# Performance work log

Measured on AMD Instinct MI355X. Metric: run time of the kernel, lower is better.

The kernel has to match this reference:

```python
import jax, jax.numpy as jnp
import numpy as np

N_NODES = 50000
N_EDGES = 800000
N_GRAPHS = 64
D = 90


def _kaiming_uniform(key, shape, fan_in):
    # kaiming_uniform_ with nonlinearity='relu': gain=sqrt(2), bound=gain*sqrt(3/fan_in)
    bound = np.sqrt(2.0) * np.sqrt(3.0 / fan_in)
    return jax.random.uniform(key, shape, jnp.float32, -bound, bound)


def setup_inputs() -> dict:
    key = jax.random.key(0)
    ks = jax.random.split(key, 16)
    x = jax.random.normal(ks[0], (N_NODES, D), jnp.float32)
    edge_index = jax.random.randint(ks[1], (2, N_EDGES), 0, N_NODES, jnp.int64)
    batch = jnp.sort(jax.random.randint(ks[2], (N_NODES,), 0, N_GRAPHS, jnp.int64))
    inp = {"x": x, "edge_index": edge_index, "batch": batch}
    # SAGEConv params: lin_l (neighbor path, with bias), lin_r (root path, no bias)
    for i, (kl, kr) in enumerate([(ks[3], ks[4]), (ks[5], ks[6]), (ks[7], ks[8])], start=1):
        inp[f"W{i}l"] = _kaiming_uniform(kl, (D, D), D)
        inp[f"b{i}"] = jnp.zeros((D,), jnp.float32)
        inp[f"W{i}r"] = _kaiming_uniform(kr, (D, D), D)
    inp["Wf1"] = _kaiming_uniform(ks[9], (32, D), D)
    inp["bf1"] = jnp.zeros((32,), jnp.float32)
    inp["Wf2"] = _kaiming_uniform(ks[10], (1, 32), 32)
    inp["bf2"] = jnp.zeros((1,), jnp.float32)
    return inp


def _sage_conv(x, src, dst, Wl, bl, Wr):
    # mean-aggregate neighbor messages x[src] at dst, then lin_l(agg) + lin_r(x)
    msg = x[src]                                           # [E, D] gather
    agg = jax.ops.segment_sum(msg, dst, num_segments=N_NODES)  # [N, D] scatter-add
    deg = jax.ops.segment_sum(jnp.ones((src.shape[0],), x.dtype), dst,
                              num_segments=N_NODES)
    agg = agg / jnp.maximum(deg, 1.0)[:, None]
    return agg @ Wl.T + bl + x @ Wr.T


def reference(x, edge_index, batch, W1l, b1, W1r, W2l, b2, W2r, W3l, b3, W3r,
              Wf1, bf1, Wf2, bf2):
    src, dst = edge_index[0], edge_index[1]
    h = jax.nn.relu(_sage_conv(x, src, dst, W1l, b1, W1r))
    h = jax.nn.relu(_sage_conv(h, src, dst, W2l, b2, W2r))
    h = jax.nn.relu(_sage_conv(h, src, dst, W3l, b3, W3r))
    # global_mean_pool over graph ids
    sums = jax.ops.segment_sum(h, batch, num_segments=N_GRAPHS)      # [G, D]
    cnts = jax.ops.segment_sum(jnp.ones((h.shape[0],), h.dtype), batch,
                               num_segments=N_GRAPHS)
    pooled = sums / jnp.maximum(cnts, 1.0)[:, None]
    h4 = jax.nn.relu(pooled @ Wf1.T + bf1)
    return h4 @ Wf2.T + bf2  # [G, 1]
```

## Files before the change

kernel.cpp:

```cpp
#include <hip/hip_runtime.h>
#include <hip/hip_bf16.h>

#define N_NODES 50000
#define N_PAD   50048
#define N_EDGES 800000
#define N_GRAPHS 64
#define D 90
#define SC  192
#define SCD 96

#define NBUCKETS 196
#define BSHIFT 8
#define BIN_EPB 4096

typedef __attribute__((ext_vector_type(8))) short bf16x8;
typedef __attribute__((ext_vector_type(4))) float f32x4;

__device__ __forceinline__ float bflo(unsigned int v) { return __uint_as_float(v << 16); }
__device__ __forceinline__ float bfhi(unsigned int v) { return __uint_as_float(v & 0xffff0000u); }
__device__ __forceinline__ unsigned short bf16bits(float f) {
    __hip_bfloat16 b = __float2bfloat16(f);
    return *(unsigned short*)&b;
}
__device__ __forceinline__ unsigned int pack2bf(float lo, float hi) {
    return (unsigned int)bf16bits(lo) | ((unsigned int)bf16bits(hi) << 16);
}

__global__ void k_prep(const float* __restrict__ x, __hip_bfloat16* __restrict__ cat,
                       const float* __restrict__ w1l, const float* __restrict__ w1r,
                       const float* __restrict__ w2l, const float* __restrict__ w2r,
                       const float* __restrict__ w3l, const float* __restrict__ w3r,
                       __hip_bfloat16* __restrict__ Wcat,
                       int* __restrict__ bcnt, float* __restrict__ pooled) {
    int idx = blockIdx.x * 256 + threadIdx.x;
    if (idx < N_PAD * 96) {
        int n = idx / 96, k = idx - n * 96;
        float v = (n < N_NODES && k < D) ? x[n * D + k] : 0.f;
        cat[n * SC + 96 + k] = __float2bfloat16(v);
    }
    if (idx < 3 * 96 * SC) {
        const int per = 96 * SC;
        int layer = idx / per, rem = idx - layer * per;
        int j = rem / SC, k = rem - j * SC;
        const float* wl = (layer == 0) ? w1l : (layer == 1) ? w2l : w3l;
        const float* wr = (layer == 0) ? w1r : (layer == 1) ? w2r : w3r;
        float v = 0.f;
        if (j < D) {
            if (k < 96) { if (k < D) v = wl[j * D + k]; }
            else        { int kk = k - 96; if (kk < D) v = wr[j * D + kk]; }
        }
        Wcat[idx] = __float2bfloat16(v);
    }
    if (idx < N_GRAPHS * D + N_GRAPHS) pooled[idx] = 0.f;
    if (idx < NBUCKETS) bcnt[idx] = 0;
}

__global__ void k_hist(const int* __restrict__ dst, int* __restrict__ bcnt) {
    __shared__ int h[NBUCKETS];
    int t = threadIdx.x;
    for (int i = t; i < NBUCKETS; i += 256) h[i] = 0;
    __syncthreads();
    int base = blockIdx.x * BIN_EPB;
    int lim = base + BIN_EPB; if (lim > N_EDGES) lim = N_EDGES;
    for (int e = base + t; e < lim; e += 256)
        atomicAdd(&h[dst[e] >> BSHIFT], 1);
    __syncthreads();
    for (int i = t; i < NBUCKETS; i += 256) {
        int c = h[i];
        if (c) atomicAdd(&bcnt[i], c);
    }
}

__global__ void k_bscan(const int* __restrict__ bcnt, int* __restrict__ bbase,
                        int* __restrict__ bcursor) {
    __shared__ int s[256];
    int t = threadIdx.x;
    int v = (t < NBUCKETS) ? bcnt[t] : 0;
    s[t] = v; __syncthreads();
    for (int o = 1; o < 256; o <<= 1) {
        int x = (t >= o) ? s[t - o] : 0;
        __syncthreads();
        s[t] += x;
        __syncthreads();
    }
    int excl = s[t] - v;
    if (t < NBUCKETS) { bbase[t] = excl; bcursor[t] = excl; }
    if (t == 255) bbase[NBUCKETS] = s[255];
}

__global__ __launch_bounds__(256) void k_bin(const int* __restrict__ src,
                                             const int* __restrict__ dst,
                                             int* __restrict__ bcursor,
                                             unsigned int* __restrict__ ebuf) {
    __shared__ int h[NBUCKETS];
    __shared__ int gb[NBUCKETS];
    int t = threadIdx.x;
    for (int i = t; i < NBUCKETS; i += 256) h[i] = 0;
    __syncthreads();
    int base = blockIdx.x * BIN_EPB;
    int sv[16], dv[16], rv[16];
    #pragma unroll
    for (int i = 0; i < 16; ++i) {
        int e = base + i * 256 + t;
        if (e < N_EDGES) {
            sv[i] = src[e];
            dv[i] = dst[e];
            rv[i] = atomicAdd(&h[dv[i] >> BSHIFT], 1);
        }
    }
    __syncthreads();
    for (int i = t; i < NBUCKETS; i += 256)
        gb[i] = h[i] ? atomicAdd(&bcursor[i], h[i]) : 0;
    __syncthreads();
    #pragma unroll
    for (int i = 0; i < 16; ++i) {
        int e = base + i * 256 + t;
        if (e < N_EDGES) {
            int b = dv[i] >> BSHIFT;
            ebuf[gb[b] + rv[i]] = (unsigned int)sv[i] | ((unsigned int)(dv[i] & 255) << 16);
        }
    }
}

__global__ __launch_bounds__(256) void k_fill2(const unsigned int* __restrict__ ebuf,
                                               const int* __restrict__ bbase,
                                               int* __restrict__ off,
                                               int* __restrict__ csr) {
    __shared__ int lcnt[256];
    __shared__ int excl[256];
    int t = threadIdx.x;
    int n0 = blockIdx.x << BSHIFT;
    int ebeg = bbase[blockIdx.x], eend = bbase[blockIdx.x + 1];
    lcnt[t] = 0;
    __syncthreads();
    for (int e = ebeg + t; e < eend; e += 256)
        atomicAdd(&lcnt[ebuf[e] >> 16], 1);
    __syncthreads();
    int v = lcnt[t];
    excl[t] = v; __syncthreads();
    for (int o = 1; o < 256; o <<= 1) {
        int x = (t >= o) ? excl[t - o] : 0;
        __syncthreads();
        excl[t] += x;
        __syncthreads();
    }
    excl[t] -= v;
    int n = n0 + t;
    if (n <= N_NODES) off[n] = ebeg + excl[t];
    lcnt[t] = 0;
    __syncthreads();
    for (int e = ebeg + t; e < eend; e += 256) {
        unsigned int u = ebuf[e];
        int li = u >> 16;
        int r = atomicAdd(&lcnt[li], 1);
        csr[ebeg + excl[li] + r] = (int)(u & 0xFFFFu);
    }
}

__global__ void k_agg(unsigned int* __restrict__ cat,
                      const int* __restrict__ off, const int* __restrict__ csr) {
    int wid  = (blockIdx.x * 256 + threadIdx.x) >> 6;
    int lane = threadIdx.x & 63;
    if (wid >= N_NODES) return;
    int beg = off[wid], end = off[wid + 1];
    int eg = lane >> 3, sl = lane & 7;
    int col = 48 + 6 * sl;

    float a[12];
    #pragma unroll
    for (int i = 0; i < 12; ++i) a[i] = 0.f;

    int e = beg + eg;
    for (; e + 8 < end; e += 16) {
        int sA = csr[e], sB = csr[e + 8];
        const unsigned int* pA = &cat[sA * SCD + col];
        const unsigned int* pB = &cat[sB * SCD + col];
        unsigned int u[6], v[6];
        #pragma unroll
        for (int i = 0; i < 6; ++i) u[i] = pA[i];
        #pragma unroll
        for (int i = 0; i < 6; ++i) v[i] = pB[i];
        #pragma unroll
        for (int i = 0; i < 6; ++i) {
            a[2 * i]     += bflo(u[i]) + bflo(v[i]);
            a[2 * i + 1] += bfhi(u[i]) + bfhi(v[i]);
        }
    }
    if (e < end) {
        const unsigned int* pA = &cat[csr[e] * SCD + col];
        unsigned int u[6];
        #pragma unroll
        for (int i = 0; i < 6; ++i) u[i] = pA[i];
        #pragma unroll
        for (int i = 0; i < 6; ++i) {
            a[2 * i]     += bflo(u[i]);
            a[2 * i + 1] += bfhi(u[i]);
        }
    }

    #pragma unroll
    for (int m = 8; m <= 32; m <<= 1) {
        #pragma unroll
        for (int i = 0; i < 12; ++i) a[i] += __shfl_xor(a[i], m);
    }

    if (eg == 0) {
        float inv = 1.0f / fmaxf((float)(end - beg), 1.0f);
        unsigned int* q = &cat[wid * SCD + 6 * sl];
        #pragma unroll
        for (int i = 0; i < 6; ++i) {
            int c0 = 12 * sl + 2 * i;
            float lo = (c0     < D) ? a[2 * i]     * inv : 0.f;
            float hi = (c0 + 1 < D) ? a[2 * i + 1] * inv : 0.f;
            q[i] = pack2bf(lo, hi);
        }
    }
}

__global__ __launch_bounds__(256) void k_gemm(
    const __hip_bfloat16* __restrict__ Acat,
    const __hip_bfloat16* __restrict__ Wcat,
    const float* __restrict__ bias,
    __hip_bfloat16* __restrict__ Hout)
{
    __shared__ float biasPad[96];
    int tid = threadIdx.x;
    if (tid < 96) biasPad[tid] = (tid < D) ? bias[tid] : 0.f;
    __syncthreads();

    int w = tid >> 6, lane = tid & 63;
    int r0 = blockIdx.x * 64 + w * 16;
    int mrow = lane & 15, kg = lane >> 4;

    const short* A = (const short*)Acat;
    const short* W = (const short*)Wcat;

    f32x4 acc[6];
    #pragma unroll
    for (int t = 0; t < 6; ++t) {
        float b = biasPad[t * 16 + mrow];
        acc[t] = (f32x4){b, b, b, b};
    }

    #pragma unroll
    for (int ks = 0; ks < 6; ++ks) {
        bf16x8 a = *(const bf16x8*)&A[(r0 + mrow) * SC + ks * 32 + kg * 8];
        #pragma unroll
        for (int t = 0; t < 6; ++t) {
            bf16x8 bfr = *(const bf16x8*)&W[(t * 16 + mrow) * SC + ks * 32 + kg * 8];
            acc[t] = __builtin_amdgcn_mfma_f32_16x16x32_bf16(a, bfr, acc[t], 0, 0, 0);
        }
    }

    int orow = r0 + kg * 4;
    #pragma unroll
    for (int t = 0; t < 6; ++t) {
        int j = t * 16 + mrow;
        #pragma unroll
        for (int v = 0; v < 4; ++v) {
            float val = (j < D) ? fmaxf(acc[t][v], 0.f) : 0.f;
            Hout[(orow + v) * SC + 96 + j] = __float2bfloat16(val);
        }
    }
}

#define POOL_WAVES 4096
__global__ void k_pool(const unsigned int* __restrict__ cat, const int* __restrict__ batch,
                       float* __restrict__ pooled, float* __restrict__ cntg) {
    int wid  = (blockIdx.x * blockDim.x + threadIdx.x) >> 6;
    int lane = threadIdx.x & 63;
    const int per = (N_NODES + POOL_WAVES - 1) / POOL_WAVES;
    int beg = wid * per;
    int end = beg + per; if (end > N_NODES) end = N_NODES;
    if (beg >= end) return;
    int cur = batch[beg];
    float a0 = 0.f, a1 = 0.f, c = 0.f;
    for (int n = beg; n < end; ++n) {
        int g = batch[n];
        if (g != cur) {
            if (lane < 45) {
                atomicAdd(&pooled[cur * D + 2 * lane], a0);
                atomicAdd(&pooled[cur * D + 2 * lane + 1], a1);
            }
            if (lane == 0) atomicAdd(&cntg[cur], c);
            a0 = a1 = c = 0.f;
            cur = g;
        }
        if (lane < 45) {
            unsigned int v = cat[n * SCD + 48 + lane];
            a0 += bflo(v);
            a1 += bfhi(v);
        }
        c += 1.f;
    }
    if (lane < 45) {
        atomicAdd(&pooled[cur * D + 2 * lane], a0);
        atomicAdd(&pooled[cur * D + 2 * lane + 1], a1);
    }
    if (lane == 0) atomicAdd(&cntg[cur], c);
}

__global__ void k_mlp(const float* __restrict__ pooled, const float* __restrict__ cntg,
                      const float* __restrict__ Wf1, const float* __restrict__ bf1,
                      const float* __restrict__ Wf2, const float* __restrict__ bf2,
                      float* __restrict__ outp) {
    __shared__ float P[N_GRAPHS][92];
    __shared__ float H4[N_GRAPHS][32];
    int tid = threadIdx.x;
    for (int idx = tid; idx < N_GRAPHS * D; idx += 256) {
        int g = idx / D, d = idx - g * D;
        P[g][d] = pooled[idx] / fmaxf(cntg[g], 1.0f);
    }
    __syncthreads();
    for (int idx = tid; idx < N_GRAPHS * 32; idx += 256) {
        int g = idx >> 5, c = idx & 31;
        float acc = bf1[c];
        for (int d = 0; d < D; ++d) acc += P[g][d] * Wf1[c * D + d];
        H4[g][c] = fmaxf(acc, 0.f);
    }
    __syncthreads();
    if (tid < N_GRAPHS) {
        float acc = bf2[0];
        #pragma unroll
        for (int c = 0; c < 32; ++c) acc += H4[tid][c] * Wf2[c];
        outp[tid] = acc;
    }
}

extern "C" void kernel_launch(void* const* d_in, const int* in_sizes, int n_in,
                              void* d_out, int out_size, void* d_ws, size_t ws_size,
                              hipStream_t stream) {
    const float* x    = (const float*)d_in[0];
    const int*   ei   = (const int*)d_in[1];
    const int*   batch= (const int*)d_in[2];
    const float* W1l  = (const float*)d_in[3];
    const float* b1   = (const float*)d_in[4];
    const float* W1r  = (const float*)d_in[5];
    const float* W2l  = (const float*)d_in[6];
    const float* b2   = (const float*)d_in[7];
    const float* W2r  = (const float*)d_in[8];
    const float* W3l  = (const float*)d_in[9];
    const float* b3   = (const float*)d_in[10];
    const float* W3r  = (const float*)d_in[11];
    const float* Wf1  = (const float*)d_in[12];
    const float* bf1  = (const float*)d_in[13];
    const float* Wf2  = (const float*)d_in[14];
    const float* bf2  = (const float*)d_in[15];
    const int* srcI = ei;
    const int* dstI = ei + N_EDGES;

    char* base = (char*)d_ws;
    size_t o = 0;
    auto alloc = [&](size_t bytes) -> void* {
        void* p = base + o;
        o = (o + bytes + 255) & ~(size_t)255;
        return p;
    };
    int*   bcnt    = (int*)alloc((size_t)NBUCKETS * 4);
    int*   bbase   = (int*)alloc((size_t)(NBUCKETS + 1) * 4);
    int*   bcursor = (int*)alloc((size_t)NBUCKETS * 4);
    int*   off     = (int*)alloc((size_t)(N_NODES + 1) * 4);
    unsigned int* ebuf = (unsigned int*)alloc((size_t)N_EDGES * 4);
    int*   csr     = (int*)alloc((size_t)N_EDGES * 4);
    __hip_bfloat16* catA = (__hip_bfloat16*)alloc((size_t)N_PAD * SC * 2);
    __hip_bfloat16* catB = (__hip_bfloat16*)alloc((size_t)N_PAD * SC * 2);
    __hip_bfloat16* Wcat = (__hip_bfloat16*)alloc((size_t)3 * 96 * SC * 2);
    float* pooled = (float*)alloc((size_t)(N_GRAPHS * D + N_GRAPHS) * 4);
    float* cntg   = pooled + N_GRAPHS * D;

    k_prep<<<(N_PAD * 96 + 255) / 256, 256, 0, stream>>>(
        x, catA, W1l, W1r, W2l, W2r, W3l, W3r, Wcat, bcnt, pooled);

    const int EB = (N_EDGES + BIN_EPB - 1) / BIN_EPB;
    k_hist<<<EB, 256, 0, stream>>>(dstI, bcnt);
    k_bscan<<<1, 256, 0, stream>>>(bcnt, bbase, bcursor);
    k_bin<<<EB, 256, 0, stream>>>(srcI, dstI, bcursor, ebuf);
    k_fill2<<<NBUCKETS, 256, 0, stream>>>(ebuf, bbase, off, csr);

    const int AGG_BLOCKS  = N_NODES / 4;
    const int GEMM_BLOCKS = N_PAD / 64;

    unsigned int* catAu = (unsigned int*)catA;
    unsigned int* catBu = (unsigned int*)catB;

    k_agg<<<AGG_BLOCKS, 256, 0, stream>>>(catAu, off, csr);
    k_gemm<<<GEMM_BLOCKS, 256, 0, stream>>>(catA, Wcat, b1, catB);
    k_agg<<<AGG_BLOCKS, 256, 0, stream>>>(catBu, off, csr);
    k_gemm<<<GEMM_BLOCKS, 256, 0, stream>>>(catB, Wcat + 96 * SC, b2, catA);
    k_agg<<<AGG_BLOCKS, 256, 0, stream>>>(catAu, off, csr);
    k_gemm<<<GEMM_BLOCKS, 256, 0, stream>>>(catA, Wcat + 2 * 96 * SC, b3, catB);

    k_pool<<<POOL_WAVES / 4, 256, 0, stream>>>(catBu, batch, pooled, cntg);
    k_mlp<<<1, 256, 0, stream>>>(pooled, cntg, Wf1, bf1, Wf2, bf2, (float*)d_out);
}
```

Measured before the change: 240.3 us.

## Fuse neighbor aggregation into per-layer GEMM kernel via shared-memory tile

Merges the separate aggregation and GEMM kernels into one k_layer kernel per SAGE layer. Each 512-thread block aggregates 64 nodes' neighbor means into a shared-memory tile, then runs MFMA with the A operand taken from shared memory for the aggregated half and from global memory for the root half. Node features shrink from a 192-wide concat buffer to a 96-wide buffer, which halves the gather footprint and drops the global write and re-read of the aggregate. In exchange, each block's GEMM must wait for its slowest node aggregation, and the larger blocks with shared memory may lower occupancy during the latency-bound gather.

```diff
diff --git a/kernel.cpp b/kernel.cpp
--- a/kernel.cpp
+++ b/kernel.cpp
@@ -6,8 +6,9 @@
 #define N_EDGES 800000
 #define N_GRAPHS 64
 #define D 90
+#define HS  96
+#define HSD 48
 #define SC  192
-#define SCD 96
 
 #define NBUCKETS 196
 #define BSHIFT 8
@@ -26,17 +27,17 @@
     return (unsigned int)bf16bits(lo) | ((unsigned int)bf16bits(hi) << 16);
 }
 
-__global__ void k_prep(const float* __restrict__ x, __hip_bfloat16* __restrict__ cat,
+__global__ void k_prep(const float* __restrict__ x, __hip_bfloat16* __restrict__ h0,
                        const float* __restrict__ w1l, const float* __restrict__ w1r,
                        const float* __restrict__ w2l, const float* __restrict__ w2r,
                        const float* __restrict__ w3l, const float* __restrict__ w3r,
                        __hip_bfloat16* __restrict__ Wcat,
                        int* __restrict__ bcnt, float* __restrict__ pooled) {
     int idx = blockIdx.x * 256 + threadIdx.x;
-    if (idx < N_PAD * 96) {
-        int n = idx / 96, k = idx - n * 96;
+    if (idx < N_PAD * HS) {
+        int n = idx / HS, k = idx - n * HS;
         float v = (n < N_NODES && k < D) ? x[n * D + k] : 0.f;
-        cat[n * SC + 96 + k] = __float2bfloat16(v);
+        h0[idx] = __float2bfloat16(v);
     }
     if (idx < 3 * 96 * SC) {
         const int per = 96 * SC;
@@ -157,115 +158,116 @@
     }
 }
 
-__global__ void k_agg(unsigned int* __restrict__ cat,
-                      const int* __restrict__ off, const int* __restrict__ csr) {
-    int wid  = (blockIdx.x * 256 + threadIdx.x) >> 6;
-    int lane = threadIdx.x & 63;
-    if (wid >= N_NODES) return;
-    int beg = off[wid], end = off[wid + 1];
-    int eg = lane >> 3, sl = lane & 7;
-    int col = 48 + 6 * sl;
-
-    float a[12];
-    #pragma unroll
-    for (int i = 0; i < 12; ++i) a[i] = 0.f;
-
-    int e = beg + eg;
-    for (; e + 8 < end; e += 16) {
-        int sA = csr[e], sB = csr[e + 8];
-        const unsigned int* pA = &cat[sA * SCD + col];
-        const unsigned int* pB = &cat[sB * SCD + col];
-        unsigned int u[6], v[6];
-        #pragma unroll
-        for (int i = 0; i < 6; ++i) u[i] = pA[i];
-        #pragma unroll
-        for (int i = 0; i < 6; ++i) v[i] = pB[i];
-        #pragma unroll
-        for (int i = 0; i < 6; ++i) {
-            a[2 * i]     += bflo(u[i]) + bflo(v[i]);
-            a[2 * i + 1] += bfhi(u[i]) + bfhi(v[i]);
-        }
-    }
-    if (e < end) {
-        const unsigned int* pA = &cat[csr[e] * SCD + col];
-        unsigned int u[6];
-        #pragma unroll
-        for (int i = 0; i < 6; ++i) u[i] = pA[i];
-        #pragma unroll
-        for (int i = 0; i < 6; ++i) {
-            a[2 * i]     += bflo(u[i]);
-            a[2 * i + 1] += bfhi(u[i]);
-        }
-    }
-
-    #pragma unroll
-    for (int m = 8; m <= 32; m <<= 1) {
-        #pragma unroll
-        for (int i = 0; i < 12; ++i) a[i] += __shfl_xor(a[i], m);
-    }
-
-    if (eg == 0) {
-        float inv = 1.0f / fmaxf((float)(end - beg), 1.0f);
-        unsigned int* q = &cat[wid * SCD + 6 * sl];
-        #pragma unroll
-        for (int i = 0; i < 6; ++i) {
-            int c0 = 12 * sl + 2 * i;
-            float lo = (c0     < D) ? a[2 * i]     * inv : 0.f;
-            float hi = (c0 + 1 < D) ? a[2 * i + 1] * inv : 0.f;
-            q[i] = pack2bf(lo, hi);
-        }
-    }
-}
-
-__global__ __launch_bounds__(256) void k_gemm(
-    const __hip_bfloat16* __restrict__ Acat,
+__global__ __launch_bounds__(512) void k_layer(
+    const unsigned int* __restrict__ hin,
     const __hip_bfloat16* __restrict__ Wcat,
     const float* __restrict__ bias,
-    __hip_bfloat16* __restrict__ Hout)
+    const int* __restrict__ off, const int* __restrict__ csr,
+    __hip_bfloat16* __restrict__ hout)
 {
+    __shared__ unsigned int aggT[64][52];
     __shared__ float biasPad[96];
     int tid = threadIdx.x;
     if (tid < 96) biasPad[tid] = (tid < D) ? bias[tid] : 0.f;
-    __syncthreads();
-
     int w = tid >> 6, lane = tid & 63;
-    int r0 = blockIdx.x * 64 + w * 16;
+
+    int eg = lane >> 3, sl = lane & 7;
+    int colw = 6 * sl;
+    for (int i = 0; i < 8; ++i) {
+        int local = w * 8 + i;
+        int node = blockIdx.x * 64 + local;
+        int beg = 0, end = 0;
+        if (node < N_NODES) { beg = off[node]; end = off[node + 1]; }
+        float a[12];
+        #pragma unroll
+        for (int q = 0; q < 12; ++q) a[q] = 0.f;
+        int e = beg + eg;
+        for (; e + 8 < end; e += 16) {
+            int sA = csr[e], sB = csr[e + 8];
+            const unsigned int* pA = &hin[sA * HSD + colw];
+            const unsigned int* pB = &hin[sB * HSD + colw];
+            unsigned int u[6], v[6];
+            #pragma unroll
+            for (int q = 0; q < 6; ++q) u[q] = pA[q];
+            #pragma unroll
+            for (int q = 0; q < 6; ++q) v[q] = pB[q];
+            #pragma unroll
+            for (int q = 0; q < 6; ++q) {
+                a[2 * q]     += bflo(u[q]) + bflo(v[q]);
+                a[2 * q + 1] += bfhi(u[q]) + bfhi(v[q]);
+            }
+        }
+        if (e < end) {
+            const unsigned int* pA = &hin[csr[e] * HSD + colw];
+            unsigned int u[6];
+            #pragma unroll
+            for (int q = 0; q < 6; ++q) u[q] = pA[q];
+            #pragma unroll
+            for (int q = 0; q < 6; ++q) {
+                a[2 * q]     += bflo(u[q]);
+                a[2 * q + 1] += bfhi(u[q]);
+            }
+        }
+        #pragma unroll
+        for (int m = 8; m <= 32; m <<= 1) {
+            #pragma unroll
+            for (int q = 0; q < 12; ++q) a[q] += __shfl_xor(a[q], m);
+        }
+        if (eg == 0) {
+            float inv = 1.0f / fmaxf((float)(end - beg), 1.0f);
+            #pragma unroll
+            for (int q = 0; q < 6; ++q) {
+                int c0 = 12 * sl + 2 * q;
+                float lo = (c0     < D) ? a[2 * q]     * inv : 0.f;
+                float hi = (c0 + 1 < D) ? a[2 * q + 1] * inv : 0.f;
+                aggT[local][colw + q] = pack2bf(lo, hi);
+            }
+        }
+    }
+    __syncthreads();
+
+    int w4 = w & 3, half = w >> 2;
     int mrow = lane & 15, kg = lane >> 4;
-
-    const short* A = (const short*)Acat;
-    const short* W = (const short*)Wcat;
-
-    f32x4 acc[6];
-    #pragma unroll
-    for (int t = 0; t < 6; ++t) {
-        float b = biasPad[t * 16 + mrow];
+    int r0 = blockIdx.x * 64 + w4 * 16;
+    int lrow = w4 * 16 + mrow;
+    const short* Wp = (const short*)Wcat;
+    const short* Hs = (const short*)hin;
+
+    f32x4 acc[3];
+    #pragma unroll
+    for (int t = 0; t < 3; ++t) {
+        int j = (half * 3 + t) * 16 + mrow;
+        float b = biasPad[j];
         acc[t] = (f32x4){b, b, b, b};
     }
 
     #pragma unroll
     for (int ks = 0; ks < 6; ++ks) {
-        bf16x8 a = *(const bf16x8*)&A[(r0 + mrow) * SC + ks * 32 + kg * 8];
-        #pragma unroll
-        for (int t = 0; t < 6; ++t) {
-            bf16x8 bfr = *(const bf16x8*)&W[(t * 16 + mrow) * SC + ks * 32 + kg * 8];
-            acc[t] = __builtin_amdgcn_mfma_f32_16x16x32_bf16(a, bfr, acc[t], 0, 0, 0);
+        bf16x8 afr;
+        if (ks < 3) afr = *(const bf16x8*)&aggT[lrow][ks * 16 + kg * 4];
+        else        afr = *(const bf16x8*)&Hs[(r0 + mrow) * HS + (ks - 3) * 32 + kg * 8];
+        #pragma unroll
+        for (int t = 0; t < 3; ++t) {
+            int j = (half * 3 + t) * 16 + mrow;
+            bf16x8 bfr = *(const bf16x8*)&Wp[j * SC + ks * 32 + kg * 8];
+            acc[t] = __builtin_amdgcn_mfma_f32_16x16x32_bf16(afr, bfr, acc[t], 0, 0, 0);
         }
     }
 
     int orow = r0 + kg * 4;
     #pragma unroll
-    for (int t = 0; t < 6; ++t) {
-        int j = t * 16 + mrow;
+    for (int t = 0; t < 3; ++t) {
+        int j = (half * 3 + t) * 16 + mrow;
         #pragma unroll
         for (int v = 0; v < 4; ++v) {
             float val = (j < D) ? fmaxf(acc[t][v], 0.f) : 0.f;
-            Hout[(orow + v) * SC + 96 + j] = __float2bfloat16(val);
+            hout[(orow + v) * HS + j] = __float2bfloat16(val);
         }
     }
 }
 
 #define POOL_WAVES 4096
-__global__ void k_pool(const unsigned int* __restrict__ cat, const int* __restrict__ batch,
+__global__ void k_pool(const unsigned int* __restrict__ h, const int* __restrict__ batch,
                        float* __restrict__ pooled, float* __restrict__ cntg) {
     int wid  = (blockIdx.x * blockDim.x + threadIdx.x) >> 6;
     int lane = threadIdx.x & 63;
@@ -287,7 +289,7 @@
             cur = g;
         }
         if (lane < 45) {
-            unsigned int v = cat[n * SCD + 48 + lane];
+            unsigned int v = h[n * HSD + lane];
             a0 += bflo(v);
             a1 += bfhi(v);
         }
@@ -362,14 +364,14 @@
     int*   off     = (int*)alloc((size_t)(N_NODES + 1) * 4);
     unsigned int* ebuf = (unsigned int*)alloc((size_t)N_EDGES * 4);
     int*   csr     = (int*)alloc((size_t)N_EDGES * 4);
-    __hip_bfloat16* catA = (__hip_bfloat16*)alloc((size_t)N_PAD * SC * 2);
-    __hip_bfloat16* catB = (__hip_bfloat16*)alloc((size_t)N_PAD * SC * 2);
+    __hip_bfloat16* hA = (__hip_bfloat16*)alloc((size_t)N_PAD * HS * 2);
+    __hip_bfloat16* hB = (__hip_bfloat16*)alloc((size_t)N_PAD * HS * 2);
     __hip_bfloat16* Wcat = (__hip_bfloat16*)alloc((size_t)3 * 96 * SC * 2);
     float* pooled = (float*)alloc((size_t)(N_GRAPHS * D + N_GRAPHS) * 4);
     float* cntg   = pooled + N_GRAPHS * D;
 
-    k_prep<<<(N_PAD * 96 + 255) / 256, 256, 0, stream>>>(
-        x, catA, W1l, W1r, W2l, W2r, W3l, W3r, Wcat, bcnt, pooled);
+    k_prep<<<(N_PAD * HS + 255) / 256, 256, 0, stream>>>(
+        x, hA, W1l, W1r, W2l, W2r, W3l, W3r, Wcat, bcnt, pooled);
 
     const int EB = (N_EDGES + BIN_EPB - 1) / BIN_EPB;
     k_hist<<<EB, 256, 0, stream>>>(dstI, bcnt);
@@ -377,19 +379,15 @@
     k_bin<<<EB, 256, 0, stream>>>(srcI, dstI, bcursor, ebuf);
     k_fill2<<<NBUCKETS, 256, 0, stream>>>(ebuf, bbase, off, csr);
 
-    const int AGG_BLOCKS  = N_NODES / 4;
-    const int GEMM_BLOCKS = N_PAD / 64;
-
-    unsigned int* catAu = (unsigned int*)catA;
-    unsigned int* catBu = (unsigned int*)catB;
-
-    k_agg<<<AGG_BLOCKS, 256, 0, stream>>>(catAu, off, csr);
-    k_gemm<<<GEMM_BLOCKS, 256, 0, stream>>>(catA, Wcat, b1, catB);
-    k_agg<<<AGG_BLOCKS, 256, 0, stream>>>(catBu, off, csr);
-    k_gemm<<<GEMM_BLOCKS, 256, 0, stream>>>(catB, Wcat + 96 * SC, b2, catA);
-    k_agg<<<AGG_BLOCKS, 256, 0, stream>>>(catAu, off, csr);
-    k_gemm<<<GEMM_BLOCKS, 256, 0, stream>>>(catA, Wcat + 2 * 96 * SC, b3, catB);
-
-    k_pool<<<POOL_WAVES / 4, 256, 0, stream>>>(catBu, batch, pooled, cntg);
+    const int LAYER_BLOCKS = N_PAD / 64;
+
+    unsigned int* hAu = (unsigned int*)hA;
+    unsigned int* hBu = (unsigned int*)hB;
+
+    k_layer<<<LAYER_BLOCKS, 512, 0, stream>>>(hAu, Wcat,            b1, off, csr, hB);
+    k_layer<<<LAYER_BLOCKS, 512, 0, stream>>>(hBu, Wcat +  96 * SC, b2, off, csr, hA);
+    k_layer<<<LAYER_BLOCKS, 512, 0, stream>>>(hAu, Wcat + 192 * SC, b3, off, csr, hB);
+
+    k_pool<<<POOL_WAVES / 4, 256, 0, stream>>>(hBu, batch, pooled, cntg);
     k_mlp<<<1, 256, 0, stream>>>(pooled, cntg, Wf1, bf1, Wf2, bf2, (float*)d_out);
 }
```

Measured after the change: 240.3 us. Within noise of the previous version (+0.0%).
